# Optimization experiments

Hardware: AMD Instinct MI355X
Metric: run time of the kernel (lower is better)

Reference implementation:

```python
import jax, jax.numpy as jnp
import numpy as np

INPUT_DIM = 1024
NUM_CLASSES = 1024
NUM_EXPERTS = 8
TOP_K = 2
HIDDEN = 128  # hard-coded in Expert


def setup_inputs() -> dict:
    key = jax.random.key(0)
    ks = jax.random.split(key, 7)
    s = 0.02
    return {
        "x": jax.random.normal(ks[0], (16384, INPUT_DIM), dtype=jnp.float32),
        "gate_w": jax.random.normal(ks[1], (INPUT_DIM, NUM_EXPERTS), dtype=jnp.float32) * s,
        "gate_b": jnp.zeros((NUM_EXPERTS,), dtype=jnp.float32),
        "w1": jax.random.normal(ks[2], (NUM_EXPERTS, INPUT_DIM, HIDDEN), dtype=jnp.float32) * s,
        "b1": jnp.zeros((NUM_EXPERTS, HIDDEN), dtype=jnp.float32),
        "w2": jax.random.normal(ks[3], (NUM_EXPERTS, HIDDEN, NUM_CLASSES), dtype=jnp.float32) * s,
        "b2": jnp.zeros((NUM_EXPERTS, NUM_CLASSES), dtype=jnp.float32),
    }


def reference(x, gate_w, gate_b, w1, b1, w2, b2):
    B = x.shape[0]
    # gating: softmax over experts, then top-k
    scores = jax.nn.softmax(x @ gate_w + gate_b, axis=1)          # [B, E]
    top_vals, top_idx = jax.lax.top_k(scores, TOP_K)              # [B, K]
    # dense all-expert compute (E small, fixed), then gather selected outputs
    h = jax.nn.relu(jnp.einsum('bi,eih->ebh', x, w1) + b1[:, None, :])   # [E, B, H]
    y = jnp.einsum('ebh,ehc->ebc', h, w2) + b2[:, None, :]               # [E, B, C]
    y = jnp.transpose(y, (1, 0, 2))                                      # [B, E, C]
    sel = jnp.take_along_axis(y, top_idx[:, :, None], axis=1)            # [B, K, C]
    output = jnp.sum(top_vals[:, :, None] * sel, axis=1)                 # [B, C]
    # gates expanded to [B, K, C] then summed over batch -> [K, C]
    gates_sum = jnp.broadcast_to(jnp.sum(top_vals, axis=0)[:, None], (TOP_K, NUM_CLASSES))
    return (output, gates_sum)
```

## Files before the change

### kernel.cpp

```cpp
#include <hip/hip_runtime.h>

#define B_ROWS  16384
#define IN_DIM  1024
#define NEXP    8
#define HID     128
#define NCLS    1024
#define NPAIR   56
#define MAXW1   520
#define MAXW2   312

typedef __attribute__((ext_vector_type(8))) short bf16x8;
typedef __attribute__((ext_vector_type(4))) float f32x4;
typedef __attribute__((ext_vector_type(4))) unsigned int u32x4;
typedef __attribute__((ext_vector_type(8))) unsigned short u16x8;

__device__ __forceinline__ unsigned short f2bf(float f) {
  union { float f; unsigned u; } v; v.f = f;
  unsigned r = v.u + 0x7FFFu + ((v.u >> 16) & 1u);
  return (unsigned short)(r >> 16);
}

__device__ __forceinline__ int sw64(int row, int sh) {
  return (row << 6) + ((((sh >> 3) ^ row) & 7) << 3) + (sh & 7);
}
__device__ __forceinline__ int sw256(int row, int sh) {
  return (row << 8) + ((((sh >> 3) ^ row) & 7) << 3) + (sh & 7) + ((sh >> 6) << 6);
}

__global__ __launch_bounds__(256) void transpose_cvt_kernel(
    const float* __restrict__ in, unsigned short* __restrict__ out,
    int R, int C) {
  __shared__ float tile[32][33];
  const int e = blockIdx.z;
  in  += (size_t)e * R * C;
  out += (size_t)e * R * C;
  const int c0 = blockIdx.x * 32, r0 = blockIdx.y * 32;
  const int tx = threadIdx.x, ty = threadIdx.y;
#pragma unroll
  for (int i = ty; i < 32; i += 8)
    tile[i][tx] = in[(size_t)(r0 + i) * C + c0 + tx];
  __syncthreads();
#pragma unroll
  for (int i = ty; i < 32; i += 8)
    out[(size_t)(c0 + i) * R + r0 + tx] = f2bf(tile[tx][i]);
}

__global__ __launch_bounds__(256) void gate_cvt(
    const float* __restrict__ x, const float* __restrict__ gw,
    const float* __restrict__ gb, unsigned short* __restrict__ xb,
    float2* __restrict__ tval, unsigned char* __restrict__ pairid) {
  __shared__ __attribute__((aligned(16))) float gws[NEXP][IN_DIM];
  const int t = threadIdx.x;
#pragma unroll
  for (int kk = 0; kk < 4; ++kk) {
    const int k = kk * 256 + t;
    const float4 g0 = *(const float4*)(gw + k * NEXP);
    const float4 g1 = *(const float4*)(gw + k * NEXP + 4);
    gws[0][k] = g0.x; gws[1][k] = g0.y; gws[2][k] = g0.z; gws[3][k] = g0.w;
    gws[4][k] = g1.x; gws[5][k] = g1.y; gws[6][k] = g1.z; gws[7][k] = g1.w;
  }
  __syncthreads();

  const int wave = t >> 6, l = t & 63;
  const int r0 = blockIdx.x * 8 + wave * 2;

  float4 xv0[4], xv1[4];
#pragma unroll
  for (int j = 0; j < 4; ++j) {
    xv0[j] = *(const float4*)(x + (size_t)r0 * IN_DIM + j * 256 + l * 4);
    xv1[j] = *(const float4*)(x + (size_t)(r0 + 1) * IN_DIM + j * 256 + l * 4);
  }

  if (xb) {
#pragma unroll
    for (int j = 0; j < 4; ++j) {
      uint2 p0, p1;
      p0.x = (unsigned)f2bf(xv0[j].x) | ((unsigned)f2bf(xv0[j].y) << 16);
      p0.y = (unsigned)f2bf(xv0[j].z) | ((unsigned)f2bf(xv0[j].w) << 16);
      p1.x = (unsigned)f2bf(xv1[j].x) | ((unsigned)f2bf(xv1[j].y) << 16);
      p1.y = (unsigned)f2bf(xv1[j].z) | ((unsigned)f2bf(xv1[j].w) << 16);
      *(uint2*)(xb + (size_t)r0 * IN_DIM + j * 256 + l * 4)       = p0;
      *(uint2*)(xb + (size_t)(r0 + 1) * IN_DIM + j * 256 + l * 4) = p1;
    }
  }

  float a0[NEXP], a1[NEXP];
#pragma unroll
  for (int e = 0; e < NEXP; ++e) { a0[e] = 0.f; a1[e] = 0.f; }
#pragma unroll
  for (int e = 0; e < NEXP; ++e) {
#pragma unroll
    for (int j = 0; j < 4; ++j) {
      const float4 g = *(const float4*)&gws[e][j * 256 + l * 4];
      a0[e] = fmaf(xv0[j].x, g.x, a0[e]); a0[e] = fmaf(xv0[j].y, g.y, a0[e]);
      a0[e] = fmaf(xv0[j].z, g.z, a0[e]); a0[e] = fmaf(xv0[j].w, g.w, a0[e]);
      a1[e] = fmaf(xv1[j].x, g.x, a1[e]); a1[e] = fmaf(xv1[j].y, g.y, a1[e]);
      a1[e] = fmaf(xv1[j].z, g.z, a1[e]); a1[e] = fmaf(xv1[j].w, g.w, a1[e]);
    }
  }
#pragma unroll
  for (int e = 0; e < NEXP; ++e) {
#pragma unroll
    for (int off = 32; off > 0; off >>= 1) {
      a0[e] += __shfl_xor(a0[e], off);
      a1[e] += __shfl_xor(a1[e], off);
    }
  }

  if (l == 0) {
#pragma unroll
    for (int rr = 0; rr < 2; ++rr) {
      const float* a = rr ? a1 : a0;
      float lg[NEXP];
#pragma unroll
      for (int e = 0; e < NEXP; ++e) lg[e] = a[e] + gb[e];
      float m = lg[0];
#pragma unroll
      for (int e = 1; e < NEXP; ++e) m = fmaxf(m, lg[e]);
      float p[NEXP], s = 0.f;
#pragma unroll
      for (int e = 0; e < NEXP; ++e) { p[e] = __expf(lg[e] - m); s += p[e]; }
      const float inv = 1.f / s;
      int   i0 = 0;  float v0 = p[0];
#pragma unroll
      for (int e = 1; e < NEXP; ++e) if (p[e] > v0) { v0 = p[e]; i0 = e; }
      int   i1 = -1; float v1 = -1.f;
#pragma unroll
      for (int e = 0; e < NEXP; ++e)
        if (e != i0 && p[e] > v1) { v1 = p[e]; i1 = e; }
      tval[r0 + rr] = make_float2(v0 * inv, v1 * inv);
      pairid[r0 + rr] = (unsigned char)(i0 * 7 + i1 - (i1 > i0 ? 1 : 0));
    }
  }
}

__global__ __launch_bounds__(256) void hist_part_kernel(
    const unsigned char* __restrict__ pairid, int* __restrict__ partials) {
  __shared__ int h[64];
  const int t = threadIdx.x;
  if (t < 64) h[t] = 0;
  __syncthreads();
  const int p  = pairid[blockIdx.x * 256 + t];
  const int ea = p / 7, rem = p % 7;
  const int eb = rem + (rem >= ea ? 1 : 0);
  atomicAdd(&h[p], 1);
  atomicAdd(&h[56 + ea], 1);
  atomicAdd(&h[56 + eb], 1);
  __syncthreads();
  if (t < 64) partials[blockIdx.x * 64 + t] = h[t];
}

__global__ void scan_kernel(const int* __restrict__ partials,
                            int* __restrict__ hist, int* __restrict__ base,
                            int* __restrict__ csr, int* __restrict__ meta) {
  const int t = threadIdx.x;
  if (t < 64) {
    int s = 0;
    for (int b = 0; b < B_ROWS / 256; ++b) s += partials[b * 64 + t];
    hist[t] = s;
  }
  __syncthreads();
  if (t != 0) return;
  int accp = 0, acce = 0;
  for (int p = 0; p < NPAIR; ++p) { base[p] = accp; csr[p] = accp; accp += hist[p]; }
  for (int e = 0; e < NEXP; ++e) {
    base[56 + e] = acce; csr[56 + e] = acce; acce += hist[56 + e];
  }
  int n = 0;
  int* w1 = meta + 2;
  for (int e = 0; e < NEXP; ++e) {
    const int tiles = (hist[56 + e] + 63) >> 6;
    for (int i = 0; i < tiles; ++i) w1[n++] = (e << 16) | i;
  }
  meta[0] = n;
  n = 0;
  int* w2 = meta + 2 + MAXW1;
  for (int p = 0; p < NPAIR; ++p) {
    const int tiles = (hist[p] + 63) >> 6;
    for (int i = 0; i < tiles; ++i) w2[n++] = (p << 16) | i;
  }
  meta[1] = n;
}

__global__ __launch_bounds__(256) void scatter_kernel(
    const unsigned char* __restrict__ pairid, int* __restrict__ csr,
    int* __restrict__ elist, int* __restrict__ plist) {
  __shared__ int h[64], lbase[64];
  const int t = threadIdx.x;
  if (t < 64) h[t] = 0;
  __syncthreads();
  const int row = blockIdx.x * 256 + t;
  const int p  = pairid[row];
  const int ea = p / 7, rem = p % 7;
  const int eb = rem + (rem >= ea ? 1 : 0);
  const int op = atomicAdd(&h[p], 1);
  const int oa = atomicAdd(&h[56 + ea], 1);
  const int ob = atomicAdd(&h[56 + eb], 1);
  __syncthreads();
  if (t < 64) lbase[t] = h[t] ? atomicAdd(&csr[t], h[t]) : 0;
  __syncthreads();
  plist[lbase[p] + op]       = row;
  elist[lbase[56 + ea] + oa] = (row << 1);
  elist[lbase[56 + eb] + ob] = (row << 1) | 1;
}

template <bool XB>
__global__ __launch_bounds__(256) void k1_hidden(
    const float* __restrict__ x, const unsigned short* __restrict__ xb,
    const unsigned short* __restrict__ w1bt, const float* __restrict__ b1,
    const float2* __restrict__ tval, const int* __restrict__ elist,
    const int* __restrict__ hist, const int* __restrict__ base,
    const int* __restrict__ meta, unsigned short* __restrict__ Hg) {
  const int b = blockIdx.x;
  if (b >= meta[0]) return;
  const int item = meta[2 + b];
  const int e = item >> 16, tile = item & 0xffff;
  const int start = tile * 64;
  const int nr = min(64, hist[56 + e] - start);

  __shared__ unsigned short As[64 * 64];
  __shared__ unsigned short Bs[128 * 64];
  __shared__ int rowl[64];

  const int t = threadIdx.x;
  if (t < 64) rowl[t] = elist[base[56 + e] + start + (t < nr ? t : 0)];
  __syncthreads();

  const int wid = t >> 6, l = t & 63;
  const int wr = wid >> 1, wc = wid & 1;
  const int lg = l >> 4,   ln = l & 15;

  f32x4 acc[2][4];
#pragma unroll
  for (int ms = 0; ms < 2; ++ms)
#pragma unroll
    for (int nf = 0; nf < 4; ++nf) acc[ms][nf] = (f32x4){0.f, 0.f, 0.f, 0.f};

  const int ai = t >> 2, aseg = t & 3;
  const float* asrcf = x + (size_t)(rowl[ai] >> 1) * IN_DIM + aseg * 16;
  const unsigned short* asrcb =
      xb + (size_t)(rowl[ai] >> 1) * IN_DIM + aseg * 16;
  const int bn = t >> 1, bhf = t & 1;
  const unsigned short* bsrc =
      w1bt + ((size_t)e * HID + bn) * IN_DIM + bhf * 32;

  for (int ks = 0; ks < 16; ++ks) {
    if constexpr (XB) {
      const u32x4* ap = (const u32x4*)(asrcb + ks * 64);
      *(u32x4*)&As[sw64(ai, aseg * 16)]     = ap[0];
      *(u32x4*)&As[sw64(ai, aseg * 16 + 8)] = ap[1];
    } else {
      const float4 f0 = *(const float4*)(asrcf + ks * 64);
      const float4 f1 = *(const float4*)(asrcf + ks * 64 + 4);
      const float4 f2 = *(const float4*)(asrcf + ks * 64 + 8);
      const float4 f3 = *(const float4*)(asrcf + ks * 64 + 12);
      u16x8 u0, u1;
      u0[0]=f2bf(f0.x); u0[1]=f2bf(f0.y); u0[2]=f2bf(f0.z); u0[3]=f2bf(f0.w);
      u0[4]=f2bf(f1.x); u0[5]=f2bf(f1.y); u0[6]=f2bf(f1.z); u0[7]=f2bf(f1.w);
      u1[0]=f2bf(f2.x); u1[1]=f2bf(f2.y); u1[2]=f2bf(f2.z); u1[3]=f2bf(f2.w);
      u1[4]=f2bf(f3.x); u1[5]=f2bf(f3.y); u1[6]=f2bf(f3.z); u1[7]=f2bf(f3.w);
      *(u16x8*)&As[sw64(ai, aseg * 16)]     = u0;
      *(u16x8*)&As[sw64(ai, aseg * 16 + 8)] = u1;
    }
    {
      const u32x4* bp = (const u32x4*)(bsrc + ks * 64);
#pragma unroll
      for (int j = 0; j < 4; ++j)
        *(u32x4*)&Bs[sw64(bn, bhf * 32 + j * 8)] = bp[j];
    }
    __syncthreads();
    bf16x8 af[2][2], bf[4][2];
#pragma unroll
    for (int ms = 0; ms < 2; ++ms)
#pragma unroll
      for (int kh = 0; kh < 2; ++kh)
        af[ms][kh] = *(const bf16x8*)&As[sw64(wr*32 + ms*16 + ln, kh*32 + lg*8)];
#pragma unroll
    for (int nf = 0; nf < 4; ++nf)
#pragma unroll
      for (int kh = 0; kh < 2; ++kh)
        bf[nf][kh] = *(const bf16x8*)&Bs[sw64(wc*64 + nf*16 + ln, kh*32 + lg*8)];
#pragma unroll
    for (int ms = 0; ms < 2; ++ms)
#pragma unroll
      for (int nf = 0; nf < 4; ++nf) {
        acc[ms][nf] = __builtin_amdgcn_mfma_f32_16x16x32_bf16(af[ms][0], bf[nf][0], acc[ms][nf], 0, 0, 0);
        acc[ms][nf] = __builtin_amdgcn_mfma_f32_16x16x32_bf16(af[ms][1], bf[nf][1], acc[ms][nf], 0, 0, 0);
      }
    __syncthreads();
  }

  float b1c[4];
#pragma unroll
  for (int nf = 0; nf < 4; ++nf) b1c[nf] = b1[e * HID + wc*64 + nf*16 + ln];

#pragma unroll
  for (int ms = 0; ms < 2; ++ms)
#pragma unroll
    for (int r = 0; r < 4; ++r) {
      const int li = wr*32 + ms*16 + lg*4 + r;
      if (li < nr) {
        const int packed = rowl[li];
        const int row = packed >> 1, slot = packed & 1;
        const float2 tv = tval[row];
        const float v = slot ? tv.y : tv.x;
#pragma unroll
        for (int nf = 0; nf < 4; ++nf) {
          const float h = fmaxf(acc[ms][nf][r] + b1c[nf], 0.f) * v;
          Hg[((size_t)row * 2 + slot) * HID + wc*64 + nf*16 + ln] = f2bf(h);
        }
      }
    }
}

__global__ __launch_bounds__(256) void k2_out(
    const unsigned short* __restrict__ Hg, const unsigned short* __restrict__ w2bt,
    const float* __restrict__ b2, const float2* __restrict__ tval,
    const int* __restrict__ plist, const int* __restrict__ hist,
    const int* __restrict__ base, const int* __restrict__ meta,
    float* __restrict__ out) {
  const int b = blockIdx.y;
  if (b >= meta[1]) return;
  const int item = meta[2 + MAXW1 + b];
  const int p = item >> 16, rt = item & 0xffff;
  const int ea = p / 7, rem = p % 7;
  const int eb = rem + (rem >= ea ? 1 : 0);
  const int start = rt * 64;
  const int nr = min(64, hist[p] - start);
  const int c0 = blockIdx.x * 128;

  __shared__ unsigned short Ah[64 * 256];
  __shared__ unsigned short Bs[128 * 64];
  __shared__ int rowl[64];
  __shared__ float2 vals[64];

  const int t = threadIdx.x;
  if (t < 64) {
    const int r = plist[base[p] + start + (t < nr ? t : 0)];
    rowl[t] = r;
    vals[t] = tval[r];
  }
  __syncthreads();

  {
    const int i = t >> 2, q = t & 3;
    const u32x4* src = (const u32x4*)(Hg + (size_t)rowl[i] * 256 + q * 64);
#pragma unroll
    for (int j = 0; j < 8; ++j)
      *(u32x4*)&Ah[sw256(i, q * 64 + j * 8)] = src[j];
  }

  const int wid = t >> 6, l = t & 63;
  const int wr = wid >> 1, wc = wid & 1;
  const int lg = l >> 4,   ln = l & 15;

  f32x4 acc[2][4];
#pragma unroll
  for (int ms = 0; ms < 2; ++ms)
#pragma unroll
    for (int nf = 0; nf < 4; ++nf) acc[ms][nf] = (f32x4){0.f, 0.f, 0.f, 0.f};

  const int bn = t >> 1, bhf = t & 1;
  for (int ks = 0; ks < 4; ++ks) {
    const int ex = (ks < 2) ? ea : eb;
    const int hb = (ks & 1) * 64;
    {
      const u32x4* bp = (const u32x4*)(
          w2bt + ((size_t)ex * NCLS + c0 + bn) * HID + hb + bhf * 32);
#pragma unroll
      for (int j = 0; j < 4; ++j)
        *(u32x4*)&Bs[sw64(bn, bhf * 32 + j * 8)] = bp[j];
    }
    __syncthreads();
    bf16x8 af[2][2], bf[4][2];
#pragma unroll
    for (int ms = 0; ms < 2; ++ms)
#pragma unroll
      for (int kh = 0; kh < 2; ++kh)
        af[ms][kh] = *(const bf16x8*)&Ah[sw256(wr*32 + ms*16 + ln, ks*64 + kh*32 + lg*8)];
#pragma unroll
    for (int nf = 0; nf < 4; ++nf)
#pragma unroll
      for (int kh = 0; kh < 2; ++kh)
        bf[nf][kh] = *(const bf16x8*)&Bs[sw64(wc*64 + nf*16 + ln, kh*32 + lg*8)];
#pragma unroll
    for (int ms = 0; ms < 2; ++ms)
#pragma unroll
      for (int nf = 0; nf < 4; ++nf) {
        acc[ms][nf] = __builtin_amdgcn_mfma_f32_16x16x32_bf16(af[ms][0], bf[nf][0], acc[ms][nf], 0, 0, 0);
        acc[ms][nf] = __builtin_amdgcn_mfma_f32_16x16x32_bf16(af[ms][1], bf[nf][1], acc[ms][nf], 0, 0, 0);
      }
    __syncthreads();
  }

  float b2a[4], b2b[4];
#pragma unroll
  for (int nf = 0; nf < 4; ++nf) {
    const int c = c0 + wc*64 + nf*16 + ln;
    b2a[nf] = b2[ea * NCLS + c];
    b2b[nf] = b2[eb * NCLS + c];
  }
#pragma unroll
  for (int ms = 0; ms < 2; ++ms)
#pragma unroll
    for (int r = 0; r < 4; ++r) {
      const int li = wr*32 + ms*16 + lg*4 + r;
      if (li < nr) {
        const int row = rowl[li];
        const float2 v = vals[li];
#pragma unroll
        for (int nf = 0; nf < 4; ++nf) {
          const int c = c0 + wc*64 + nf*16 + ln;
          out[(size_t)row * NCLS + c] = acc[ms][nf][r] + v.x * b2a[nf] + v.y * b2b[nf];
        }
      }
    }
}

__global__ __launch_bounds__(256) void gates_out_kernel(
    const float2* __restrict__ tval, float* __restrict__ out) {
  __shared__ float r0[256], r1[256];
  float s0 = 0.f, s1 = 0.f;
  for (int i = threadIdx.x; i < B_ROWS; i += 256) {
    const float2 v = tval[i];
    s0 += v.x; s1 += v.y;
  }
  r0[threadIdx.x] = s0; r1[threadIdx.x] = s1;
  __syncthreads();
#pragma unroll
  for (int s = 128; s > 0; s >>= 1) {
    if (threadIdx.x < s) {
      r0[threadIdx.x] += r0[threadIdx.x + s];
      r1[threadIdx.x] += r1[threadIdx.x + s];
    }
    __syncthreads();
  }
  const float g0 = r0[0], g1 = r1[0];
  float* gout = out + (size_t)B_ROWS * NCLS;
  for (int c = threadIdx.x; c < NCLS; c += 256) {
    gout[c]        = g0;
    gout[NCLS + c] = g1;
  }
}

extern "C" void kernel_launch(void* const* d_in, const int* in_sizes, int n_in,
                              void* d_out, int out_size, void* d_ws, size_t ws_size,
                              hipStream_t stream) {
  const float* x   = (const float*)d_in[0];
  const float* gw  = (const float*)d_in[1];
  const float* gb  = (const float*)d_in[2];
  const float* w1  = (const float*)d_in[3];
  const float* b1  = (const float*)d_in[4];
  const float* w2  = (const float*)d_in[5];
  const float* b2  = (const float*)d_in[6];
  float* out = (float*)d_out;

  char* ws = (char*)d_ws;
  int*            hist     = (int*)(ws);
  int*            base     = (int*)(ws + 256);
  int*            csr      = (int*)(ws + 512);
  int*            meta     = (int*)(ws + 768);
  int*            partials = (int*)(ws + 4352);
  unsigned char*  pairid   = (unsigned char*)(ws + 20736);
  float2*         tval     = (float2*)(ws + 37120);
  int*            elist    = (int*)(ws + 168192);
  int*            plist    = (int*)(ws + 299264);
  unsigned short* w1bt     = (unsigned short*)(ws + 364800);
  unsigned short* w2bt     = (unsigned short*)(ws + 2461952);
  unsigned short* Hg       = (unsigned short*)(ws + 4559104);
  const bool use_xb = (ws_size >= (size_t)46502144);
  unsigned short* xb = use_xb ? (unsigned short*)(ws + 12947712) : nullptr;

  dim3 tb(32, 8);
  transpose_cvt_kernel<<<dim3(HID / 32, IN_DIM / 32, NEXP), tb, 0, stream>>>(
      w1, w1bt, IN_DIM, HID);
  transpose_cvt_kernel<<<dim3(NCLS / 32, HID / 32, NEXP), tb, 0, stream>>>(
      w2, w2bt, HID, NCLS);

  gate_cvt<<<B_ROWS / 8, 256, 0, stream>>>(x, gw, gb, xb, tval, pairid);
  hist_part_kernel<<<B_ROWS / 256, 256, 0, stream>>>(pairid, partials);
  scan_kernel<<<1, 64, 0, stream>>>(partials, hist, base, csr, meta);
  scatter_kernel<<<B_ROWS / 256, 256, 0, stream>>>(pairid, csr, elist, plist);

  if (use_xb)
    k1_hidden<true><<<MAXW1, 256, 0, stream>>>(x, xb, w1bt, b1, tval, elist,
                                               hist, base, meta, Hg);
  else
    k1_hidden<false><<<MAXW1, 256, 0, stream>>>(x, xb, w1bt, b1, tval, elist,
                                                hist, base, meta, Hg);
  k2_out<<<dim3(NCLS / 128, MAXW2), 256, 0, stream>>>(Hg, w2bt, b2, tval, plist,
                                                      hist, base, meta, out);

  gates_out_kernel<<<1, 256, 0, stream>>>(tval, out);
}
```

Baseline: 142.1 us.

## Merge prep kernels, fold gate-sum into hist/scan, register-prefetch GEMM tiles

Combines the gating/x-conversion kernel and both weight transpose-convert kernels into a single launch that dispatches on block index. The gate-sum reduction moves into the histogram and scan kernels, which removes the separate single-block gates kernel. Both expert GEMM loops now prefetch the next K-slice into registers while the current slice is computed, overlapping global loads with MFMA work. This saves launch overhead and load latency at the cost of more registers and a larger shared buffer in the merged prep kernel.

```diff
diff --git a/kernel.cpp b/kernel.cpp
--- a/kernel.cpp
+++ b/kernel.cpp
@@ -9,6 +9,10 @@
 #define MAXW1   520
 #define MAXW2   312
 
+#define GATE_BLOCKS (B_ROWS / 8)
+#define W1T_BLOCKS  (NEXP * (IN_DIM / 32) * (HID / 32))
+#define W2T_BLOCKS  (NEXP * (HID / 32) * (NCLS / 32))
+
 typedef __attribute__((ext_vector_type(8))) short bf16x8;
 typedef __attribute__((ext_vector_type(4))) float f32x4;
 typedef __attribute__((ext_vector_type(4))) unsigned int u32x4;
@@ -27,139 +31,179 @@
   return (row << 8) + ((((sh >> 3) ^ row) & 7) << 3) + (sh & 7) + ((sh >> 6) << 6);
 }
 
-__global__ __launch_bounds__(256) void transpose_cvt_kernel(
-    const float* __restrict__ in, unsigned short* __restrict__ out,
-    int R, int C) {
-  __shared__ float tile[32][33];
-  const int e = blockIdx.z;
-  in  += (size_t)e * R * C;
-  out += (size_t)e * R * C;
-  const int c0 = blockIdx.x * 32, r0 = blockIdx.y * 32;
-  const int tx = threadIdx.x, ty = threadIdx.y;
-#pragma unroll
-  for (int i = ty; i < 32; i += 8)
-    tile[i][tx] = in[(size_t)(r0 + i) * C + c0 + tx];
-  __syncthreads();
-#pragma unroll
-  for (int i = ty; i < 32; i += 8)
-    out[(size_t)(c0 + i) * R + r0 + tx] = f2bf(tile[tx][i]);
-}
-
-__global__ __launch_bounds__(256) void gate_cvt(
+__global__ __launch_bounds__(256) void prep_kernel(
     const float* __restrict__ x, const float* __restrict__ gw,
-    const float* __restrict__ gb, unsigned short* __restrict__ xb,
+    const float* __restrict__ gb, const float* __restrict__ w1,
+    const float* __restrict__ w2, unsigned short* __restrict__ xb,
+    unsigned short* __restrict__ w1bt, unsigned short* __restrict__ w2bt,
     float2* __restrict__ tval, unsigned char* __restrict__ pairid) {
-  __shared__ __attribute__((aligned(16))) float gws[NEXP][IN_DIM];
+  __shared__ __attribute__((aligned(16))) unsigned char pmem[NEXP * IN_DIM * 4];
+  const int bid = blockIdx.x;
   const int t = threadIdx.x;
-#pragma unroll
-  for (int kk = 0; kk < 4; ++kk) {
-    const int k = kk * 256 + t;
-    const float4 g0 = *(const float4*)(gw + k * NEXP);
-    const float4 g1 = *(const float4*)(gw + k * NEXP + 4);
-    gws[0][k] = g0.x; gws[1][k] = g0.y; gws[2][k] = g0.z; gws[3][k] = g0.w;
-    gws[4][k] = g1.x; gws[5][k] = g1.y; gws[6][k] = g1.z; gws[7][k] = g1.w;
-  }
-  __syncthreads();
-
-  const int wave = t >> 6, l = t & 63;
-  const int r0 = blockIdx.x * 8 + wave * 2;
-
-  float4 xv0[4], xv1[4];
-#pragma unroll
-  for (int j = 0; j < 4; ++j) {
-    xv0[j] = *(const float4*)(x + (size_t)r0 * IN_DIM + j * 256 + l * 4);
-    xv1[j] = *(const float4*)(x + (size_t)(r0 + 1) * IN_DIM + j * 256 + l * 4);
-  }
-
-  if (xb) {
+
+  if (bid < GATE_BLOCKS) {
+    float (*gws)[IN_DIM] = (float(*)[IN_DIM])pmem;
+#pragma unroll
+    for (int kk = 0; kk < 4; ++kk) {
+      const int k = kk * 256 + t;
+      const float4 g0 = *(const float4*)(gw + k * NEXP);
+      const float4 g1 = *(const float4*)(gw + k * NEXP + 4);
+      gws[0][k] = g0.x; gws[1][k] = g0.y; gws[2][k] = g0.z; gws[3][k] = g0.w;
+      gws[4][k] = g1.x; gws[5][k] = g1.y; gws[6][k] = g1.z; gws[7][k] = g1.w;
+    }
+    __syncthreads();
+
+    const int wave = t >> 6, l = t & 63;
+    const int r0 = bid * 8 + wave * 2;
+
+    float4 xv0[4], xv1[4];
 #pragma unroll
     for (int j = 0; j < 4; ++j) {
-      uint2 p0, p1;
-      p0.x = (unsigned)f2bf(xv0[j].x) | ((unsigned)f2bf(xv0[j].y) << 16);
-      p0.y = (unsigned)f2bf(xv0[j].z) | ((unsigned)f2bf(xv0[j].w) << 16);
-      p1.x = (unsigned)f2bf(xv1[j].x) | ((unsigned)f2bf(xv1[j].y) << 16);
-      p1.y = (unsigned)f2bf(xv1[j].z) | ((unsigned)f2bf(xv1[j].w) << 16);
-      *(uint2*)(xb + (size_t)r0 * IN_DIM + j * 256 + l * 4)       = p0;
-      *(uint2*)(xb + (size_t)(r0 + 1) * IN_DIM + j * 256 + l * 4) = p1;
-    }
-  }
-
-  float a0[NEXP], a1[NEXP];
-#pragma unroll
-  for (int e = 0; e < NEXP; ++e) { a0[e] = 0.f; a1[e] = 0.f; }
-#pragma unroll
-  for (int e = 0; e < NEXP; ++e) {
-#pragma unroll
-    for (int j = 0; j < 4; ++j) {
-      const float4 g = *(const float4*)&gws[e][j * 256 + l * 4];
-      a0[e] = fmaf(xv0[j].x, g.x, a0[e]); a0[e] = fmaf(xv0[j].y, g.y, a0[e]);
-      a0[e] = fmaf(xv0[j].z, g.z, a0[e]); a0[e] = fmaf(xv0[j].w, g.w, a0[e]);
-      a1[e] = fmaf(xv1[j].x, g.x, a1[e]); a1[e] = fmaf(xv1[j].y, g.y, a1[e]);
-      a1[e] = fmaf(xv1[j].z, g.z, a1[e]); a1[e] = fmaf(xv1[j].w, g.w, a1[e]);
-    }
-  }
-#pragma unroll
-  for (int e = 0; e < NEXP; ++e) {
-#pragma unroll
-    for (int off = 32; off > 0; off >>= 1) {
-      a0[e] += __shfl_xor(a0[e], off);
-      a1[e] += __shfl_xor(a1[e], off);
-    }
-  }
-
-  if (l == 0) {
-#pragma unroll
-    for (int rr = 0; rr < 2; ++rr) {
-      const float* a = rr ? a1 : a0;
-      float lg[NEXP];
-#pragma unroll
-      for (int e = 0; e < NEXP; ++e) lg[e] = a[e] + gb[e];
-      float m = lg[0];
-#pragma unroll
-      for (int e = 1; e < NEXP; ++e) m = fmaxf(m, lg[e]);
-      float p[NEXP], s = 0.f;
-#pragma unroll
-      for (int e = 0; e < NEXP; ++e) { p[e] = __expf(lg[e] - m); s += p[e]; }
-      const float inv = 1.f / s;
-      int   i0 = 0;  float v0 = p[0];
-#pragma unroll
-      for (int e = 1; e < NEXP; ++e) if (p[e] > v0) { v0 = p[e]; i0 = e; }
-      int   i1 = -1; float v1 = -1.f;
-#pragma unroll
-      for (int e = 0; e < NEXP; ++e)
-        if (e != i0 && p[e] > v1) { v1 = p[e]; i1 = e; }
-      tval[r0 + rr] = make_float2(v0 * inv, v1 * inv);
-      pairid[r0 + rr] = (unsigned char)(i0 * 7 + i1 - (i1 > i0 ? 1 : 0));
-    }
+      xv0[j] = *(const float4*)(x + (size_t)r0 * IN_DIM + j * 256 + l * 4);
+      xv1[j] = *(const float4*)(x + (size_t)(r0 + 1) * IN_DIM + j * 256 + l * 4);
+    }
+
+    if (xb) {
+#pragma unroll
+      for (int j = 0; j < 4; ++j) {
+        uint2 p0, p1;
+        p0.x = (unsigned)f2bf(xv0[j].x) | ((unsigned)f2bf(xv0[j].y) << 16);
+        p0.y = (unsigned)f2bf(xv0[j].z) | ((unsigned)f2bf(xv0[j].w) << 16);
+        p1.x = (unsigned)f2bf(xv1[j].x) | ((unsigned)f2bf(xv1[j].y) << 16);
+        p1.y = (unsigned)f2bf(xv1[j].z) | ((unsigned)f2bf(xv1[j].w) << 16);
+        *(uint2*)(xb + (size_t)r0 * IN_DIM + j * 256 + l * 4)       = p0;
+        *(uint2*)(xb + (size_t)(r0 + 1) * IN_DIM + j * 256 + l * 4) = p1;
+      }
+    }
+
+    float a0[NEXP], a1[NEXP];
+#pragma unroll
+    for (int e = 0; e < NEXP; ++e) { a0[e] = 0.f; a1[e] = 0.f; }
+#pragma unroll
+    for (int e = 0; e < NEXP; ++e) {
+#pragma unroll
+      for (int j = 0; j < 4; ++j) {
+        const float4 g = *(const float4*)&gws[e][j * 256 + l * 4];
+        a0[e] = fmaf(xv0[j].x, g.x, a0[e]); a0[e] = fmaf(xv0[j].y, g.y, a0[e]);
+        a0[e] = fmaf(xv0[j].z, g.z, a0[e]); a0[e] = fmaf(xv0[j].w, g.w, a0[e]);
+        a1[e] = fmaf(xv1[j].x, g.x, a1[e]); a1[e] = fmaf(xv1[j].y, g.y, a1[e]);
+        a1[e] = fmaf(xv1[j].z, g.z, a1[e]); a1[e] = fmaf(xv1[j].w, g.w, a1[e]);
+      }
+    }
+#pragma unroll
+    for (int e = 0; e < NEXP; ++e) {
+#pragma unroll
+      for (int off = 32; off > 0; off >>= 1) {
+        a0[e] += __shfl_xor(a0[e], off);
+        a1[e] += __shfl_xor(a1[e], off);
+      }
+    }
+
+    if (l == 0) {
+#pragma unroll
+      for (int rr = 0; rr < 2; ++rr) {
+        const float* a = rr ? a1 : a0;
+        float lg[NEXP];
+#pragma unroll
+        for (int e = 0; e < NEXP; ++e) lg[e] = a[e] + gb[e];
+        float m = lg[0];
+#pragma unroll
+        for (int e = 1; e < NEXP; ++e) m = fmaxf(m, lg[e]);
+        float p[NEXP], s = 0.f;
+#pragma unroll
+        for (int e = 0; e < NEXP; ++e) { p[e] = __expf(lg[e] - m); s += p[e]; }
+        const float inv = 1.f / s;
+        int   i0 = 0;  float v0 = p[0];
+#pragma unroll
+        for (int e = 1; e < NEXP; ++e) if (p[e] > v0) { v0 = p[e]; i0 = e; }
+        int   i1 = -1; float v1 = -1.f;
+#pragma unroll
+        for (int e = 0; e < NEXP; ++e)
+          if (e != i0 && p[e] > v1) { v1 = p[e]; i1 = e; }
+        tval[r0 + rr] = make_float2(v0 * inv, v1 * inv);
+        pairid[r0 + rr] = (unsigned char)(i0 * 7 + i1 - (i1 > i0 ? 1 : 0));
+      }
+    }
+  } else {
+    float (*tile)[33] = (float(*)[33])pmem;
+    const float* src; unsigned short* dst;
+    int R, C, r0, c0, e;
+    if (bid < GATE_BLOCKS + W1T_BLOCKS) {
+      const int b1 = bid - GATE_BLOCKS;
+      e = b1 >> 7; const int rem = b1 & 127;
+      R = IN_DIM; C = HID;
+      c0 = (rem & 3) * 32; r0 = (rem >> 2) * 32;
+      src = w1; dst = w1bt;
+    } else {
+      const int b2 = bid - GATE_BLOCKS - W1T_BLOCKS;
+      e = b2 >> 7; const int rem = b2 & 127;
+      R = HID; C = NCLS;
+      c0 = (rem & 31) * 32; r0 = (rem >> 5) * 32;
+      src = w2; dst = w2bt;
+    }
+    src += (size_t)e * R * C;
+    dst += (size_t)e * R * C;
+    const int tx = t & 31, ty = t >> 5;
+#pragma unroll
+    for (int i = ty; i < 32; i += 8)
+      tile[i][tx] = src[(size_t)(r0 + i) * C + c0 + tx];
+    __syncthreads();
+#pragma unroll
+    for (int i = ty; i < 32; i += 8)
+      dst[(size_t)(c0 + i) * R + r0 + tx] = f2bf(tile[tx][i]);
   }
 }
 
 __global__ __launch_bounds__(256) void hist_part_kernel(
-    const unsigned char* __restrict__ pairid, int* __restrict__ partials) {
+    const unsigned char* __restrict__ pairid, const float2* __restrict__ tval,
+    int* __restrict__ partials, float2* __restrict__ psum) {
   __shared__ int h[64];
+  __shared__ float s0a[256], s1a[256];
   const int t = threadIdx.x;
   if (t < 64) h[t] = 0;
   __syncthreads();
-  const int p  = pairid[blockIdx.x * 256 + t];
+  const int row = blockIdx.x * 256 + t;
+  const int p  = pairid[row];
   const int ea = p / 7, rem = p % 7;
   const int eb = rem + (rem >= ea ? 1 : 0);
   atomicAdd(&h[p], 1);
   atomicAdd(&h[56 + ea], 1);
   atomicAdd(&h[56 + eb], 1);
-  __syncthreads();
+  const float2 v = tval[row];
+  s0a[t] = v.x; s1a[t] = v.y;
+  __syncthreads();
+#pragma unroll
+  for (int s = 128; s > 0; s >>= 1) {
+    if (t < s) { s0a[t] += s0a[t + s]; s1a[t] += s1a[t + s]; }
+    __syncthreads();
+  }
   if (t < 64) partials[blockIdx.x * 64 + t] = h[t];
+  if (t == 0) psum[blockIdx.x] = make_float2(s0a[0], s1a[0]);
 }
 
 __global__ void scan_kernel(const int* __restrict__ partials,
+                            const float2* __restrict__ psum,
                             int* __restrict__ hist, int* __restrict__ base,
-                            int* __restrict__ csr, int* __restrict__ meta) {
+                            int* __restrict__ csr, int* __restrict__ meta,
+                            float* __restrict__ out) {
   const int t = threadIdx.x;
+  __shared__ float gg[2];
   if (t < 64) {
     int s = 0;
     for (int b = 0; b < B_ROWS / 256; ++b) s += partials[b * 64 + t];
     hist[t] = s;
   }
-  __syncthreads();
+  if (t == 0) {
+    float g0 = 0.f, g1 = 0.f;
+    for (int b = 0; b < B_ROWS / 256; ++b) { g0 += psum[b].x; g1 += psum[b].y; }
+    gg[0] = g0; gg[1] = g1;
+  }
+  __syncthreads();
+  float* gout = out + (size_t)B_ROWS * NCLS;
+  for (int c = t; c < NCLS; c += 64) {
+    gout[c]        = gg[0];
+    gout[NCLS + c] = gg[1];
+  }
   if (t != 0) return;
   int accp = 0, acce = 0;
   for (int p = 0; p < NPAIR; ++p) { base[p] = accp; csr[p] = accp; accp += hist[p]; }
@@ -244,50 +288,91 @@
   const unsigned short* bsrc =
       w1bt + ((size_t)e * HID + bn) * IN_DIM + bhf * 32;
 
-  for (int ks = 0; ks < 16; ++ks) {
-    if constexpr (XB) {
-      const u32x4* ap = (const u32x4*)(asrcb + ks * 64);
-      *(u32x4*)&As[sw64(ai, aseg * 16)]     = ap[0];
-      *(u32x4*)&As[sw64(ai, aseg * 16 + 8)] = ap[1];
-    } else {
-      const float4 f0 = *(const float4*)(asrcf + ks * 64);
-      const float4 f1 = *(const float4*)(asrcf + ks * 64 + 4);
-      const float4 f2 = *(const float4*)(asrcf + ks * 64 + 8);
-      const float4 f3 = *(const float4*)(asrcf + ks * 64 + 12);
-      u16x8 u0, u1;
-      u0[0]=f2bf(f0.x); u0[1]=f2bf(f0.y); u0[2]=f2bf(f0.z); u0[3]=f2bf(f0.w);
-      u0[4]=f2bf(f1.x); u0[5]=f2bf(f1.y); u0[6]=f2bf(f1.z); u0[7]=f2bf(f1.w);
-      u1[0]=f2bf(f2.x); u1[1]=f2bf(f2.y); u1[2]=f2bf(f2.z); u1[3]=f2bf(f2.w);
-      u1[4]=f2bf(f3.x); u1[5]=f2bf(f3.y); u1[6]=f2bf(f3.z); u1[7]=f2bf(f3.w);
-      *(u16x8*)&As[sw64(ai, aseg * 16)]     = u0;
-      *(u16x8*)&As[sw64(ai, aseg * 16 + 8)] = u1;
-    }
+  if constexpr (XB) {
+    u32x4 areg[2], breg[4];
     {
-      const u32x4* bp = (const u32x4*)(bsrc + ks * 64);
+      const u32x4* ap = (const u32x4*)(asrcb);
+      areg[0] = ap[0]; areg[1] = ap[1];
+      const u32x4* bp = (const u32x4*)(bsrc);
+#pragma unroll
+      for (int j = 0; j < 4; ++j) breg[j] = bp[j];
+    }
+    for (int ks = 0; ks < 16; ++ks) {
+      *(u32x4*)&As[sw64(ai, aseg * 16)]     = areg[0];
+      *(u32x4*)&As[sw64(ai, aseg * 16 + 8)] = areg[1];
 #pragma unroll
       for (int j = 0; j < 4; ++j)
-        *(u32x4*)&Bs[sw64(bn, bhf * 32 + j * 8)] = bp[j];
-    }
-    __syncthreads();
-    bf16x8 af[2][2], bf[4][2];
-#pragma unroll
-    for (int ms = 0; ms < 2; ++ms)
-#pragma unroll
-      for (int kh = 0; kh < 2; ++kh)
-        af[ms][kh] = *(const bf16x8*)&As[sw64(wr*32 + ms*16 + ln, kh*32 + lg*8)];
-#pragma unroll
-    for (int nf = 0; nf < 4; ++nf)
-#pragma unroll
-      for (int kh = 0; kh < 2; ++kh)
-        bf[nf][kh] = *(const bf16x8*)&Bs[sw64(wc*64 + nf*16 + ln, kh*32 + lg*8)];
-#pragma unroll
-    for (int ms = 0; ms < 2; ++ms)
-#pragma unroll
-      for (int nf = 0; nf < 4; ++nf) {
-        acc[ms][nf] = __builtin_amdgcn_mfma_f32_16x16x32_bf16(af[ms][0], bf[nf][0], acc[ms][nf], 0, 0, 0);
-        acc[ms][nf] = __builtin_amdgcn_mfma_f32_16x16x32_bf16(af[ms][1], bf[nf][1], acc[ms][nf], 0, 0, 0);
-      }
-    __syncthreads();
+        *(u32x4*)&Bs[sw64(bn, bhf * 32 + j * 8)] = breg[j];
+      __syncthreads();
+      if (ks < 15) {
+        const u32x4* ap = (const u32x4*)(asrcb + (ks + 1) * 64);
+        areg[0] = ap[0]; areg[1] = ap[1];
+        const u32x4* bp = (const u32x4*)(bsrc + (ks + 1) * 64);
+#pragma unroll
+        for (int j = 0; j < 4; ++j) breg[j] = bp[j];
+      }
+      bf16x8 af[2][2], bf[4][2];
+#pragma unroll
+      for (int ms = 0; ms < 2; ++ms)
+#pragma unroll
+        for (int kh = 0; kh < 2; ++kh)
+          af[ms][kh] = *(const bf16x8*)&As[sw64(wr*32 + ms*16 + ln, kh*32 + lg*8)];
+#pragma unroll
+      for (int nf = 0; nf < 4; ++nf)
+#pragma unroll
+        for (int kh = 0; kh < 2; ++kh)
+          bf[nf][kh] = *(const bf16x8*)&Bs[sw64(wc*64 + nf*16 + ln, kh*32 + lg*8)];
+#pragma unroll
+      for (int ms = 0; ms < 2; ++ms)
+#pragma unroll
+        for (int nf = 0; nf < 4; ++nf) {
+          acc[ms][nf] = __builtin_amdgcn_mfma_f32_16x16x32_bf16(af[ms][0], bf[nf][0], acc[ms][nf], 0, 0, 0);
+          acc[ms][nf] = __builtin_amdgcn_mfma_f32_16x16x32_bf16(af[ms][1], bf[nf][1], acc[ms][nf], 0, 0, 0);
+        }
+      __syncthreads();
+    }
+  } else {
+    for (int ks = 0; ks < 16; ++ks) {
+      {
+        const float4 f0 = *(const float4*)(asrcf + ks * 64);
+        const float4 f1 = *(const float4*)(asrcf + ks * 64 + 4);
+        const float4 f2 = *(const float4*)(asrcf + ks * 64 + 8);
+        const float4 f3 = *(const float4*)(asrcf + ks * 64 + 12);
+        u16x8 u0, u1;
+        u0[0]=f2bf(f0.x); u0[1]=f2bf(f0.y); u0[2]=f2bf(f0.z); u0[3]=f2bf(f0.w);
+        u0[4]=f2bf(f1.x); u0[5]=f2bf(f1.y); u0[6]=f2bf(f1.z); u0[7]=f2bf(f1.w);
+        u1[0]=f2bf(f2.x); u1[1]=f2bf(f2.y); u1[2]=f2bf(f2.z); u1[3]=f2bf(f2.w);
+        u1[4]=f2bf(f3.x); u1[5]=f2bf(f3.y); u1[6]=f2bf(f3.z); u1[7]=f2bf(f3.w);
+        *(u16x8*)&As[sw64(ai, aseg * 16)]     = u0;
+        *(u16x8*)&As[sw64(ai, aseg * 16 + 8)] = u1;
+      }
+      {
+        const u32x4* bp = (const u32x4*)(bsrc + ks * 64);
+#pragma unroll
+        for (int j = 0; j < 4; ++j)
+          *(u32x4*)&Bs[sw64(bn, bhf * 32 + j * 8)] = bp[j];
+      }
+      __syncthreads();
+      bf16x8 af[2][2], bf[4][2];
+#pragma unroll
+      for (int ms = 0; ms < 2; ++ms)
+#pragma unroll
+        for (int kh = 0; kh < 2; ++kh)
+          af[ms][kh] = *(const bf16x8*)&As[sw64(wr*32 + ms*16 + ln, kh*32 + lg*8)];
+#pragma unroll
+      for (int nf = 0; nf < 4; ++nf)
+#pragma unroll
+        for (int kh = 0; kh < 2; ++kh)
+          bf[nf][kh] = *(const bf16x8*)&Bs[sw64(wc*64 + nf*16 + ln, kh*32 + lg*8)];
+#pragma unroll
+      for (int ms = 0; ms < 2; ++ms)
+#pragma unroll
+        for (int nf = 0; nf < 4; ++nf) {
+          acc[ms][nf] = __builtin_amdgcn_mfma_f32_16x16x32_bf16(af[ms][0], bf[nf][0], acc[ms][nf], 0, 0, 0);
+          acc[ms][nf] = __builtin_amdgcn_mfma_f32_16x16x32_bf16(af[ms][1], bf[nf][1], acc[ms][nf], 0, 0, 0);
+        }
+      __syncthreads();
+    }
   }
 
   float b1c[4];
@@ -361,17 +446,27 @@
     for (int nf = 0; nf < 4; ++nf) acc[ms][nf] = (f32x4){0.f, 0.f, 0.f, 0.f};
 
   const int bn = t >> 1, bhf = t & 1;
+  u32x4 breg[4];
+  {
+    const u32x4* bp = (const u32x4*)(
+        w2bt + ((size_t)ea * NCLS + c0 + bn) * HID + bhf * 32);
+#pragma unroll
+    for (int j = 0; j < 4; ++j) breg[j] = bp[j];
+  }
+#pragma unroll
   for (int ks = 0; ks < 4; ++ks) {
-    const int ex = (ks < 2) ? ea : eb;
-    const int hb = (ks & 1) * 64;
-    {
+#pragma unroll
+    for (int j = 0; j < 4; ++j)
+      *(u32x4*)&Bs[sw64(bn, bhf * 32 + j * 8)] = breg[j];
+    __syncthreads();
+    if (ks < 3) {
+      const int exn = (ks + 1 < 2) ? ea : eb;
+      const int hbn = ((ks + 1) & 1) * 64;
       const u32x4* bp = (const u32x4*)(
-          w2bt + ((size_t)ex * NCLS + c0 + bn) * HID + hb + bhf * 32);
-#pragma unroll
-      for (int j = 0; j < 4; ++j)
-        *(u32x4*)&Bs[sw64(bn, bhf * 32 + j * 8)] = bp[j];
-    }
-    __syncthreads();
+          w2bt + ((size_t)exn * NCLS + c0 + bn) * HID + hbn + bhf * 32);
+#pragma unroll
+      for (int j = 0; j < 4; ++j) breg[j] = bp[j];
+    }
     bf16x8 af[2][2], bf[4][2];
 #pragma unroll
     for (int ms = 0; ms < 2; ++ms)
@@ -415,32 +510,6 @@
         }
       }
     }
-}
-
-__global__ __launch_bounds__(256) void gates_out_kernel(
-    const float2* __restrict__ tval, float* __restrict__ out) {
-  __shared__ float r0[256], r1[256];
-  float s0 = 0.f, s1 = 0.f;
-  for (int i = threadIdx.x; i < B_ROWS; i += 256) {
-    const float2 v = tval[i];
-    s0 += v.x; s1 += v.y;
-  }
-  r0[threadIdx.x] = s0; r1[threadIdx.x] = s1;
-  __syncthreads();
-#pragma unroll
-  for (int s = 128; s > 0; s >>= 1) {
-    if (threadIdx.x < s) {
-      r0[threadIdx.x] += r0[threadIdx.x + s];
-      r1[threadIdx.x] += r1[threadIdx.x + s];
-    }
-    __syncthreads();
-  }
-  const float g0 = r0[0], g1 = r1[0];
-  float* gout = out + (size_t)B_ROWS * NCLS;
-  for (int c = threadIdx.x; c < NCLS; c += 256) {
-    gout[c]        = g0;
-    gout[NCLS + c] = g1;
-  }
 }
 
 extern "C" void kernel_launch(void* const* d_in, const int* in_sizes, int n_in,
@@ -461,25 +530,21 @@
   int*            csr      = (int*)(ws + 512);
   int*            meta     = (int*)(ws + 768);
   int*            partials = (int*)(ws + 4352);
-  unsigned char*  pairid   = (unsigned char*)(ws + 20736);
-  float2*         tval     = (float2*)(ws + 37120);
-  int*            elist    = (int*)(ws + 168192);
-  int*            plist    = (int*)(ws + 299264);
-  unsigned short* w1bt     = (unsigned short*)(ws + 364800);
-  unsigned short* w2bt     = (unsigned short*)(ws + 2461952);
-  unsigned short* Hg       = (unsigned short*)(ws + 4559104);
-  const bool use_xb = (ws_size >= (size_t)46502144);
-  unsigned short* xb = use_xb ? (unsigned short*)(ws + 12947712) : nullptr;
-
-  dim3 tb(32, 8);
-  transpose_cvt_kernel<<<dim3(HID / 32, IN_DIM / 32, NEXP), tb, 0, stream>>>(
-      w1, w1bt, IN_DIM, HID);
-  transpose_cvt_kernel<<<dim3(NCLS / 32, HID / 32, NEXP), tb, 0, stream>>>(
-      w2, w2bt, HID, NCLS);
-
-  gate_cvt<<<B_ROWS / 8, 256, 0, stream>>>(x, gw, gb, xb, tval, pairid);
-  hist_part_kernel<<<B_ROWS / 256, 256, 0, stream>>>(pairid, partials);
-  scan_kernel<<<1, 64, 0, stream>>>(partials, hist, base, csr, meta);
+  float2*         psum     = (float2*)(ws + 20736);
+  unsigned char*  pairid   = (unsigned char*)(ws + 21248);
+  float2*         tval     = (float2*)(ws + 37632);
+  int*            elist    = (int*)(ws + 168704);
+  int*            plist    = (int*)(ws + 299776);
+  unsigned short* w1bt     = (unsigned short*)(ws + 365312);
+  unsigned short* w2bt     = (unsigned short*)(ws + 2462464);
+  unsigned short* Hg       = (unsigned short*)(ws + 4559616);
+  const bool use_xb = (ws_size >= (size_t)46502656);
+  unsigned short* xb = use_xb ? (unsigned short*)(ws + 12948224) : nullptr;
+
+  prep_kernel<<<GATE_BLOCKS + W1T_BLOCKS + W2T_BLOCKS, 256, 0, stream>>>(
+      x, gw, gb, w1, w2, xb, w1bt, w2bt, tval, pairid);
+  hist_part_kernel<<<B_ROWS / 256, 256, 0, stream>>>(pairid, tval, partials, psum);
+  scan_kernel<<<1, 64, 0, stream>>>(partials, psum, hist, base, csr, meta, out);
   scatter_kernel<<<B_ROWS / 256, 256, 0, stream>>>(pairid, csr, elist, plist);
 
   if (use_xb)
@@ -490,6 +555,4 @@
                                                 hist, base, meta, Hg);
   k2_out<<<dim3(NCLS / 128, MAXW2), 256, 0, stream>>>(Hg, w2bt, b2, tval, plist,
                                                       hist, base, meta, out);
-
-  gates_out_kernel<<<1, 256, 0, stream>>>(tval, out);
-}
+}
```

After: 118.0 us. -17.0%, faster.
